# Kernel tuning notes

Measured on AMD Instinct MI355X. Metric: run time of the kernel, lower is better.

The kernel has to match this reference:

```python
import jax, jax.numpy as jnp
import numpy as np

D = 1024  # input_dim


def setup_inputs() -> dict:
    key = jax.random.key(0)
    ks = jax.random.split(key, 7)
    scale = 1.0 / np.sqrt(D)
    x = jax.random.normal(ks[0], (4, D, 2048), dtype=jnp.float32)
    Wq = jax.random.uniform(ks[1], (D, D), jnp.float32, -scale, scale)
    bq = jax.random.uniform(ks[2], (D,), jnp.float32, -scale, scale)
    Wk = jax.random.uniform(ks[3], (D, D), jnp.float32, -scale, scale)
    bk = jax.random.uniform(ks[4], (D,), jnp.float32, -scale, scale)
    Wv = jax.random.uniform(ks[5], (D, D), jnp.float32, -scale, scale)
    bv = jax.random.uniform(ks[6], (D,), jnp.float32, -scale, scale)
    return {"x": x, "Wq": Wq, "bq": bq, "Wk": Wk, "bk": bk, "Wv": Wv, "bv": bv}


def reference(x, Wq, bq, Wk, bk, Wv, bv):
    # x: [B, D, S] -> [B, S, D]
    xt = jnp.transpose(x, (0, 2, 1))
    # torch nn.Linear: y = x @ W^T + b
    q = jnp.einsum('bsd,ed->bse', xt, Wq) + bq
    k = jnp.einsum('bsd,ed->bse', xt, Wk) + bk
    v = jnp.einsum('bsd,ed->bse', xt, Wv) + bv
    scores = jnp.einsum('bse,bte->bst', q, k) / jnp.sqrt(jnp.float32(D))
    attn = jax.nn.softmax(scores, axis=2)
    out = jnp.einsum('bst,bte->bse', attn, v)  # [B, S, D]
    return out
```

## Files before the change

### kernel.cpp

```cpp
#include <hip/hip_runtime.h>
#include <stdint.h>

typedef unsigned short us16;
typedef unsigned short us8  __attribute__((ext_vector_type(8)));
typedef unsigned short us4v __attribute__((ext_vector_type(4)));
typedef __bf16         bf16x8 __attribute__((ext_vector_type(8)));
typedef float          f32x4  __attribute__((ext_vector_type(4)));

__device__ __forceinline__ us16 f2bf(float f) {
    union { float f; unsigned int u; } c; c.f = f;
    unsigned int u = (c.u + 0x7fffu + ((c.u >> 16) & 1u)) >> 16;
    return (us16)u;
}
__device__ __forceinline__ float bf2f(us16 h) {
    union { unsigned int u; float f; } c; c.u = ((unsigned int)h) << 16;
    return c.f;
}

__device__ __forceinline__ void async16(const us16* g, us16* l) {
    __builtin_amdgcn_global_load_lds(
        (const __attribute__((address_space(1))) unsigned int*)g,
        (__attribute__((address_space(3))) unsigned int*)l,
        16, 0, 0);
}

template <bool OUT_F32>
__device__ __forceinline__ void gemm_core(
        const us16* __restrict__ A, const us16* __restrict__ B,
        void* __restrict__ C, const float* __restrict__ bias, int biasmode,
        int M, int K, int x, int y, us16* lsA, us16* lsB) {
    const int m0 = x * 128, n0 = y * 128;
    const int tid = threadIdx.x;
    const int lane = tid & 63, wid = tid >> 6;
    const int l15 = lane & 15, quad = lane >> 4;
    const int wm = (wid & 1) * 64, wn = (wid >> 1) * 64;

    f32x4 acc[4][4] = {};

    const int srow = wid * 32 + (lane >> 3);
    const int sc8 = (lane & 7) ^ ((lane >> 3) & 7);
    const us16* Ap = A + (size_t)(m0 + srow) * K + sc8 * 8;
    const us16* Bp = B + (size_t)(n0 + srow) * K + sc8 * 8;
    us16* ldsAw = &lsA[(wid * 32) * 64];
    us16* ldsBw = &lsB[(wid * 32) * 64];

    for (int kb = 0; kb < K; kb += 64) {
        __syncthreads();
#pragma unroll
        for (int c = 0; c < 4; c++) {
            async16(Ap + kb + (size_t)(c * 8) * K, ldsAw + c * 8 * 64);
            async16(Bp + kb + (size_t)(c * 8) * K, ldsBw + c * 8 * 64);
        }
        __syncthreads();
#pragma unroll
        for (int ks = 0; ks < 2; ks++) {
            bf16x8 af[4], bfr[4];
#pragma unroll
            for (int i = 0; i < 4; i++) {
                const int ra = wm + i * 16 + l15;
                const int rb = wn + i * 16 + l15;
                const int pa = ((ks * 4 + quad) ^ (ra & 7)) * 8;
                const int pb = ((ks * 4 + quad) ^ (rb & 7)) * 8;
                af[i]  = *(const bf16x8*)(&lsA[ra * 64 + pa]);
                bfr[i] = *(const bf16x8*)(&lsB[rb * 64 + pb]);
            }
#pragma unroll
            for (int i = 0; i < 4; i++)
#pragma unroll
                for (int j = 0; j < 4; j++)
                    acc[i][j] = __builtin_amdgcn_mfma_f32_16x16x32_bf16(af[i], bfr[j], acc[i][j], 0, 0, 0);
        }
    }

#pragma unroll
    for (int i = 0; i < 4; i++) {
        const int mb = m0 + wm + i * 16 + quad * 4;
        float b0 = 0.f, b1 = 0.f, b2 = 0.f, b3 = 0.f;
        if (biasmode == 1) {
            float4 bv4 = *(const float4*)(bias + mb);
            b0 = bv4.x; b1 = bv4.y; b2 = bv4.z; b3 = bv4.w;
        }
#pragma unroll
        for (int j = 0; j < 4; j++) {
            const int n = n0 + wn + j * 16 + l15;
            const float bn = (biasmode == 2) ? bias[n] : 0.0f;
            f32x4 v = acc[i][j];
            const float o0 = v[0] + b0 + bn, o1 = v[1] + b1 + bn;
            const float o2 = v[2] + b2 + bn, o3 = v[3] + b3 + bn;
            if (OUT_F32) {
                float4 st; st.x = o0; st.y = o1; st.z = o2; st.w = o3;
                *(float4*)((float*)C + (size_t)n * M + mb) = st;
            } else {
                us4v st = { f2bf(o0), f2bf(o1), f2bf(o2), f2bf(o3) };
                *(us4v*)((us16*)C + (size_t)n * M + mb) = st;
            }
        }
    }
}

__device__ __forceinline__ void strip_xy(int lin, int gy, int& x, int& y) {
    const int within = lin & (4 * gy - 1);
    x = (lin / (4 * gy)) * 4 + (within & 3);
    y = within >> 2;
}

__global__ __launch_bounds__(256)
void prep(const float* __restrict__ x, us16* __restrict__ xt,
          const float* __restrict__ wq, const float* __restrict__ wk,
          const float* __restrict__ wv, us16* __restrict__ wb) {
    __shared__ us16 tile[64 * 65];
    const int id = blockIdx.x;
    const int t = threadIdx.x;
    if (id < 2048) {
        const int s0 = (id & 31) * 64, d0 = ((id >> 5) & 15) * 64, b = id >> 9;
        const float* xp = x + ((size_t)b * 1024 + d0) * 2048 + s0;
        const int r = t >> 4, c4 = t & 15;
#pragma unroll
        for (int i = 0; i < 4; i++) {
            float4 v = *(const float4*)(xp + (size_t)(r + 16 * i) * 2048 + c4 * 4);
            const int d = r + 16 * i;
            tile[(c4 * 4 + 0) * 65 + d] = f2bf(v.x);
            tile[(c4 * 4 + 1) * 65 + d] = f2bf(v.y);
            tile[(c4 * 4 + 2) * 65 + d] = f2bf(v.z);
            tile[(c4 * 4 + 3) * 65 + d] = f2bf(v.w);
        }
        __syncthreads();
        us16* op = xt + ((size_t)b * 2048 + s0) * 1024 + d0;
#pragma unroll
        for (int i = 0; i < 2; i++) {
            const int u = t + 256 * i;
            const int s = u >> 3, c8 = u & 7;
            us8 o;
#pragma unroll
            for (int j = 0; j < 8; j++) o[j] = tile[s * 65 + c8 * 8 + j];
            *(us8*)(op + (size_t)s * 1024 + c8 * 8) = o;
        }
    } else {
        const int cid = id - 2048;
        const int mb = cid >> 10;
        const float* src = (mb == 0) ? wq : (mb == 1) ? wk : wv;
        const size_t off = ((size_t)(cid & 1023) * 256 + t) * 4;
        float4 v = *(const float4*)(src + off);
        us4v o = { f2bf(v.x), f2bf(v.y), f2bf(v.z), f2bf(v.w) };
        *(us4v*)(wb + (size_t)mb * 1048576 + off) = o;
    }
}

__global__ __launch_bounds__(256)
void qkv(const us16* __restrict__ Wb, const us16* __restrict__ XT,
         us16* __restrict__ Qb, us16* __restrict__ Kb, us16* __restrict__ VT,
         const float* __restrict__ bq, const float* __restrict__ bk,
         const float* __restrict__ bv) {
    __shared__ us16 lsA[128 * 64];
    __shared__ us16 lsB[128 * 64];
    const int id = blockIdx.x;
    const long long sXT = 2097152;
    if (id < 1024) {
        const int z = id >> 7, zz = z & 3;
        const bool isK = z >= 4;
        int x, y; strip_xy(id & 127, 16, x, y);
        const us16* A = Wb + (isK ? 1048576 : 0);
        const us16* B = XT + (size_t)zz * sXT;
        us16* C = (isK ? Kb : Qb) + (size_t)zz * sXT;
        gemm_core<false>(A, B, (void*)C, isK ? bk : bq, 1, 1024, 1024, x, y, lsA, lsB);
    } else {
        const int id2 = id - 1024;
        const int z = id2 >> 7;
        int x, y; strip_xy(id2 & 127, 8, x, y);
        const us16* A = XT + (size_t)z * sXT;
        us16* C = VT + (size_t)z * sXT;
        gemm_core<false>(A, Wb + 2097152, (void*)C, bv, 2, 2048, 1024, x, y, lsA, lsB);
    }
}

__global__ __launch_bounds__(256)
void scores_k(const us16* __restrict__ Kb, const us16* __restrict__ Qb,
              us16* __restrict__ Sb) {
    __shared__ us16 lsA[128 * 64];
    __shared__ us16 lsB[128 * 64];
    const long long sXT = 2097152, sSS = 4194304;
    const int z = blockIdx.z;
    int x, y; strip_xy(blockIdx.x + 16 * blockIdx.y, 16, x, y);
    gemm_core<false>(Kb + (size_t)z * sXT, Qb + (size_t)z * sXT,
                     (void*)(Sb + (size_t)z * sSS), nullptr, 0,
                     2048, 1024, x, y, lsA, lsB);
}

__global__ __launch_bounds__(256)
void out_k(const us16* __restrict__ VT, const us16* __restrict__ Sb,
           float* __restrict__ out) {
    __shared__ us16 lsA[128 * 64];
    __shared__ us16 lsB[128 * 64];
    const long long sXT = 2097152, sSS = 4194304;
    const int z = blockIdx.z;
    int x, y; strip_xy(blockIdx.x + 8 * blockIdx.y, 16, x, y);
    gemm_core<true>(VT + (size_t)z * sXT, Sb + (size_t)z * sSS,
                    (void*)(out + (size_t)z * sXT), nullptr, 0,
                    1024, 2048, x, y, lsA, lsB);
}

__global__ __launch_bounds__(256)
void softmax_inplace(us16* __restrict__ S) {
    const float scale = 0.03125f;
    us16* p = S + (size_t)blockIdx.x * 2048;
    const int t = threadIdx.x;
    us8 v = *(const us8*)(p + t * 8);
    float x[8];
#pragma unroll
    for (int i = 0; i < 8; i++) x[i] = bf2f(v[i]) * scale;

    float m = x[0];
#pragma unroll
    for (int i = 1; i < 8; i++) m = fmaxf(m, x[i]);
#pragma unroll
    for (int off = 1; off < 64; off <<= 1) m = fmaxf(m, __shfl_xor(m, off, 64));
    __shared__ float red[4];
    __shared__ float red2[4];
    if ((t & 63) == 0) red[t >> 6] = m;
    __syncthreads();
    m = fmaxf(fmaxf(red[0], red[1]), fmaxf(red[2], red[3]));

    float s = 0.f;
#pragma unroll
    for (int i = 0; i < 8; i++) { x[i] = __expf(x[i] - m); s += x[i]; }
#pragma unroll
    for (int off = 1; off < 64; off <<= 1) s += __shfl_xor(s, off, 64);
    if ((t & 63) == 0) red2[t >> 6] = s;
    __syncthreads();
    s = red2[0] + red2[1] + red2[2] + red2[3];
    const float inv = 1.0f / s;

    us8 o;
#pragma unroll
    for (int i = 0; i < 8; i++) o[i] = f2bf(x[i] * inv);
    *(us8*)(p + t * 8) = o;
}

extern "C" void kernel_launch(void* const* d_in, const int* in_sizes, int n_in,
                              void* d_out, int out_size, void* d_ws, size_t ws_size,
                              hipStream_t stream) {
    const float* x  = (const float*)d_in[0];
    const float* Wq = (const float*)d_in[1];
    const float* bq = (const float*)d_in[2];
    const float* Wk = (const float*)d_in[3];
    const float* bk = (const float*)d_in[4];
    const float* Wv = (const float*)d_in[5];
    const float* bv = (const float*)d_in[6];
    float* out = (float*)d_out;
    char* ws = (char*)d_ws;

    const size_t SZ = 16777216;
    us16* Qb = (us16*)(ws);
    us16* Kb = (us16*)(ws + SZ);
    us16* VT = (us16*)(ws + 2 * SZ);
    us16* XT = (us16*)(ws + 3 * SZ);
    us16* Wb = (us16*)(ws + 4 * SZ);
    us16* Sb = (us16*)(ws + 3 * SZ);

    dim3 blk(256, 1, 1);

    prep<<<dim3(5120, 1, 1), blk, 0, stream>>>(x, XT, Wq, Wk, Wv, Wb);
    qkv<<<dim3(1536, 1, 1), blk, 0, stream>>>(Wb, XT, Qb, Kb, VT, bq, bk, bv);
    scores_k<<<dim3(16, 16, 4), blk, 0, stream>>>(Kb, Qb, Sb);
    softmax_inplace<<<dim3(8192, 1, 1), blk, 0, stream>>>(Sb);
    out_k<<<dim3(8, 16, 4), blk, 0, stream>>>(VT, Sb, out);
}
```

Baseline: 271.8 us.

## Double-buffer GEMM LDS tiles with 32-wide K steps to overlap loads and MFMA

Replaces the single-buffered 64-wide K tile with two 32-wide LDS buffers. The async global-to-LDS load of the next tile is issued before computing on the current one, so there is one barrier per step instead of a load-wait-compute pattern. The XOR swizzle is reworked for 32-element rows. This is meant to hide global load latency behind MFMA work, at the cost of twice as many barriers per unit of K and smaller per-step compute.

```diff
diff --git a/kernel.cpp b/kernel.cpp
--- a/kernel.cpp
+++ b/kernel.cpp
@@ -24,52 +24,67 @@
         16, 0, 0);
 }
 
+__device__ __forceinline__ void stage32(const us16* Ap, const us16* Bp,
+                                        us16* la, us16* lb, int K) {
+    async16(Ap, la);
+    async16(Ap + (size_t)16 * K, la + 16 * 32);
+    async16(Bp, lb);
+    async16(Bp + (size_t)16 * K, lb + 16 * 32);
+}
+
+__device__ __forceinline__ void compute32(const us16* La, const us16* Lb,
+        f32x4 (&acc)[4][4], int wm, int wn, int l15, int fsl) {
+    bf16x8 af[4], bfr[4];
+#pragma unroll
+    for (int i = 0; i < 4; i++) {
+        af[i]  = *(const bf16x8*)(&La[(wm + i * 16 + l15) * 32 + fsl]);
+        bfr[i] = *(const bf16x8*)(&Lb[(wn + i * 16 + l15) * 32 + fsl]);
+    }
+#pragma unroll
+    for (int i = 0; i < 4; i++)
+#pragma unroll
+        for (int j = 0; j < 4; j++)
+            acc[i][j] = __builtin_amdgcn_mfma_f32_16x16x32_bf16(af[i], bfr[j], acc[i][j], 0, 0, 0);
+}
+
 template <bool OUT_F32>
 __device__ __forceinline__ void gemm_core(
         const us16* __restrict__ A, const us16* __restrict__ B,
         void* __restrict__ C, const float* __restrict__ bias, int biasmode,
-        int M, int K, int x, int y, us16* lsA, us16* lsB) {
+        int M, int K, int x, int y, us16* ls) {
     const int m0 = x * 128, n0 = y * 128;
     const int tid = threadIdx.x;
     const int lane = tid & 63, wid = tid >> 6;
     const int l15 = lane & 15, quad = lane >> 4;
     const int wm = (wid & 1) * 64, wn = (wid >> 1) * 64;
+    const int fsl = (quad ^ ((l15 >> 1) & 3)) * 8;
 
     f32x4 acc[4][4] = {};
 
-    const int srow = wid * 32 + (lane >> 3);
-    const int sc8 = (lane & 7) ^ ((lane >> 3) & 7);
-    const us16* Ap = A + (size_t)(m0 + srow) * K + sc8 * 8;
-    const us16* Bp = B + (size_t)(n0 + srow) * K + sc8 * 8;
-    us16* ldsAw = &lsA[(wid * 32) * 64];
-    us16* ldsBw = &lsB[(wid * 32) * 64];
-
-    for (int kb = 0; kb < K; kb += 64) {
+    const int srow = lane >> 2;
+    const int sc4 = (lane & 3) ^ ((lane >> 3) & 3);
+    const us16* Ap = A + (size_t)(m0 + wid * 32 + srow) * K + sc4 * 8;
+    const us16* Bp = B + (size_t)(n0 + wid * 32 + srow) * K + sc4 * 8;
+    us16* lA0 = ls + (wid * 32) * 32;
+    us16* lB0 = ls + 4096 + (wid * 32) * 32;
+    us16* lA1 = lA0 + 8192;
+    us16* lB1 = lB0 + 8192;
+    const us16* La0 = ls;
+    const us16* Lb0 = ls + 4096;
+    const us16* La1 = ls + 8192;
+    const us16* Lb1 = ls + 12288;
+
+    stage32(Ap, Bp, lA0, lB0, K);
+    const int nIter = K >> 5;
+    int kb = 32;
+    for (int i = 0; i < nIter; i += 2) {
         __syncthreads();
-#pragma unroll
-        for (int c = 0; c < 4; c++) {
-            async16(Ap + kb + (size_t)(c * 8) * K, ldsAw + c * 8 * 64);
-            async16(Bp + kb + (size_t)(c * 8) * K, ldsBw + c * 8 * 64);
-        }
+        if (i + 1 < nIter) stage32(Ap + kb, Bp + kb, lA1, lB1, K);
+        compute32(La0, Lb0, acc, wm, wn, l15, fsl);
         __syncthreads();
-#pragma unroll
-        for (int ks = 0; ks < 2; ks++) {
-            bf16x8 af[4], bfr[4];
-#pragma unroll
-            for (int i = 0; i < 4; i++) {
-                const int ra = wm + i * 16 + l15;
-                const int rb = wn + i * 16 + l15;
-                const int pa = ((ks * 4 + quad) ^ (ra & 7)) * 8;
-                const int pb = ((ks * 4 + quad) ^ (rb & 7)) * 8;
-                af[i]  = *(const bf16x8*)(&lsA[ra * 64 + pa]);
-                bfr[i] = *(const bf16x8*)(&lsB[rb * 64 + pb]);
-            }
-#pragma unroll
-            for (int i = 0; i < 4; i++)
-#pragma unroll
-                for (int j = 0; j < 4; j++)
-                    acc[i][j] = __builtin_amdgcn_mfma_f32_16x16x32_bf16(af[i], bfr[j], acc[i][j], 0, 0, 0);
-        }
+        if (i + 2 < nIter) stage32(Ap + kb + 32, Bp + kb + 32, lA0, lB0, K);
+        compute32(La1, Lb1, acc, wm, wn, l15, fsl);
+        kb += 64;
     }
 
 #pragma unroll
@@ -151,8 +166,7 @@
          us16* __restrict__ Qb, us16* __restrict__ Kb, us16* __restrict__ VT,
          const float* __restrict__ bq, const float* __restrict__ bk,
          const float* __restrict__ bv) {
-    __shared__ us16 lsA[128 * 64];
-    __shared__ us16 lsB[128 * 64];
+    __shared__ us16 ls[16384];
     const int id = blockIdx.x;
     const long long sXT = 2097152;
     if (id < 1024) {
@@ -162,41 +176,39 @@
         const us16* A = Wb + (isK ? 1048576 : 0);
         const us16* B = XT + (size_t)zz * sXT;
         us16* C = (isK ? Kb : Qb) + (size_t)zz * sXT;
-        gemm_core<false>(A, B, (void*)C, isK ? bk : bq, 1, 1024, 1024, x, y, lsA, lsB);
+        gemm_core<false>(A, B, (void*)C, isK ? bk : bq, 1, 1024, 1024, x, y, ls);
     } else {
         const int id2 = id - 1024;
         const int z = id2 >> 7;
         int x, y; strip_xy(id2 & 127, 8, x, y);
         const us16* A = XT + (size_t)z * sXT;
         us16* C = VT + (size_t)z * sXT;
-        gemm_core<false>(A, Wb + 2097152, (void*)C, bv, 2, 2048, 1024, x, y, lsA, lsB);
+        gemm_core<false>(A, Wb + 2097152, (void*)C, bv, 2, 2048, 1024, x, y, ls);
     }
 }
 
 __global__ __launch_bounds__(256)
 void scores_k(const us16* __restrict__ Kb, const us16* __restrict__ Qb,
               us16* __restrict__ Sb) {
-    __shared__ us16 lsA[128 * 64];
-    __shared__ us16 lsB[128 * 64];
+    __shared__ us16 ls[16384];
     const long long sXT = 2097152, sSS = 4194304;
     const int z = blockIdx.z;
     int x, y; strip_xy(blockIdx.x + 16 * blockIdx.y, 16, x, y);
     gemm_core<false>(Kb + (size_t)z * sXT, Qb + (size_t)z * sXT,
                      (void*)(Sb + (size_t)z * sSS), nullptr, 0,
-                     2048, 1024, x, y, lsA, lsB);
+                     2048, 1024, x, y, ls);
 }
 
 __global__ __launch_bounds__(256)
 void out_k(const us16* __restrict__ VT, const us16* __restrict__ Sb,
            float* __restrict__ out) {
-    __shared__ us16 lsA[128 * 64];
-    __shared__ us16 lsB[128 * 64];
+    __shared__ us16 ls[16384];
     const long long sXT = 2097152, sSS = 4194304;
     const int z = blockIdx.z;
     int x, y; strip_xy(blockIdx.x + 8 * blockIdx.y, 16, x, y);
     gemm_core<true>(VT + (size_t)z * sXT, Sb + (size_t)z * sSS,
                     (void*)(out + (size_t)z * sXT), nullptr, 0,
-                    1024, 2048, x, y, lsA, lsB);
+                    1024, 2048, x, y, ls);
 }
 
 __global__ __launch_bounds__(256)
```

After: 290.7 us. 7.0% more time.

## Fuse softmax into scores epilogue and defer normalization to output GEMM

Applied to the files above, without the earlier changes.

Removes the separate softmax kernel. The scores GEMM epilogue now applies exp to the scaled scores, stores them as bf16, and accumulates per-row sums into a global buffer with atomics. The output GEMM divides by those sums in its epilogue. This saves a full read and write of the score matrix, but it drops the max subtraction, so exp could overflow for larger logits, and it adds a memset plus atomic traffic.

```diff
diff --git a/kernel.cpp b/kernel.cpp
--- a/kernel.cpp
+++ b/kernel.cpp
@@ -24,10 +24,11 @@
         16, 0, 0);
 }
 
-template <bool OUT_F32>
+template <int EPI>
 __device__ __forceinline__ void gemm_core(
         const us16* __restrict__ A, const us16* __restrict__ B,
-        void* __restrict__ C, const float* __restrict__ bias, int biasmode,
+        void* __restrict__ C, const float* __restrict__ bias,
+        float* __restrict__ L,
         int M, int K, int x, int y, us16* lsA, us16* lsB) {
     const int m0 = x * 128, n0 = y * 128;
     const int tid = threadIdx.x;
@@ -72,26 +73,58 @@
         }
     }
 
+    if (EPI == 2) {
+        const float scale = 0.03125f;
+        float rs[4] = {0.f, 0.f, 0.f, 0.f};
+#pragma unroll
+        for (int i = 0; i < 4; i++) {
+            const int mb = m0 + wm + i * 16 + quad * 4;
+#pragma unroll
+            for (int j = 0; j < 4; j++) {
+                const int n = n0 + wn + j * 16 + l15;
+                f32x4 v = acc[i][j];
+                const float e0 = __expf(v[0] * scale), e1 = __expf(v[1] * scale);
+                const float e2 = __expf(v[2] * scale), e3 = __expf(v[3] * scale);
+                rs[j] += (e0 + e1) + (e2 + e3);
+                us4v st = { f2bf(e0), f2bf(e1), f2bf(e2), f2bf(e3) };
+                *(us4v*)((us16*)C + (size_t)n * M + mb) = st;
+            }
+        }
+#pragma unroll
+        for (int j = 0; j < 4; j++) {
+            rs[j] += __shfl_xor(rs[j], 16, 64);
+            rs[j] += __shfl_xor(rs[j], 32, 64);
+        }
+        if (quad == 0) {
+#pragma unroll
+            for (int j = 0; j < 4; j++)
+                atomicAdd(&L[n0 + wn + j * 16 + l15], rs[j]);
+        }
+        return;
+    }
+
 #pragma unroll
     for (int i = 0; i < 4; i++) {
         const int mb = m0 + wm + i * 16 + quad * 4;
         float b0 = 0.f, b1 = 0.f, b2 = 0.f, b3 = 0.f;
-        if (biasmode == 1) {
+        if (EPI == 0) {
             float4 bv4 = *(const float4*)(bias + mb);
             b0 = bv4.x; b1 = bv4.y; b2 = bv4.z; b3 = bv4.w;
         }
 #pragma unroll
         for (int j = 0; j < 4; j++) {
             const int n = n0 + wn + j * 16 + l15;
-            const float bn = (biasmode == 2) ? bias[n] : 0.0f;
             f32x4 v = acc[i][j];
-            const float o0 = v[0] + b0 + bn, o1 = v[1] + b1 + bn;
-            const float o2 = v[2] + b2 + bn, o3 = v[3] + b3 + bn;
-            if (OUT_F32) {
-                float4 st; st.x = o0; st.y = o1; st.z = o2; st.w = o3;
+            if (EPI == 3) {
+                const float inv = 1.0f / L[n];
+                float4 st;
+                st.x = v[0] * inv; st.y = v[1] * inv;
+                st.z = v[2] * inv; st.w = v[3] * inv;
                 *(float4*)((float*)C + (size_t)n * M + mb) = st;
             } else {
-                us4v st = { f2bf(o0), f2bf(o1), f2bf(o2), f2bf(o3) };
+                const float bn = (EPI == 1) ? bias[n] : 0.0f;
+                us4v st = { f2bf(v[0] + b0 + bn), f2bf(v[1] + b1 + bn),
+                            f2bf(v[2] + b2 + bn), f2bf(v[3] + b3 + bn) };
                 *(us4v*)((us16*)C + (size_t)n * M + mb) = st;
             }
         }
@@ -162,78 +195,41 @@
         const us16* A = Wb + (isK ? 1048576 : 0);
         const us16* B = XT + (size_t)zz * sXT;
         us16* C = (isK ? Kb : Qb) + (size_t)zz * sXT;
-        gemm_core<false>(A, B, (void*)C, isK ? bk : bq, 1, 1024, 1024, x, y, lsA, lsB);
+        gemm_core<0>(A, B, (void*)C, isK ? bk : bq, nullptr, 1024, 1024, x, y, lsA, lsB);
     } else {
         const int id2 = id - 1024;
         const int z = id2 >> 7;
         int x, y; strip_xy(id2 & 127, 8, x, y);
         const us16* A = XT + (size_t)z * sXT;
         us16* C = VT + (size_t)z * sXT;
-        gemm_core<false>(A, Wb + 2097152, (void*)C, bv, 2, 2048, 1024, x, y, lsA, lsB);
+        gemm_core<1>(A, Wb + 2097152, (void*)C, bv, nullptr, 2048, 1024, x, y, lsA, lsB);
     }
 }
 
 __global__ __launch_bounds__(256)
 void scores_k(const us16* __restrict__ Kb, const us16* __restrict__ Qb,
-              us16* __restrict__ Sb) {
+              us16* __restrict__ Sb, float* __restrict__ L) {
     __shared__ us16 lsA[128 * 64];
     __shared__ us16 lsB[128 * 64];
     const long long sXT = 2097152, sSS = 4194304;
     const int z = blockIdx.z;
     int x, y; strip_xy(blockIdx.x + 16 * blockIdx.y, 16, x, y);
-    gemm_core<false>(Kb + (size_t)z * sXT, Qb + (size_t)z * sXT,
-                     (void*)(Sb + (size_t)z * sSS), nullptr, 0,
-                     2048, 1024, x, y, lsA, lsB);
+    gemm_core<2>(Kb + (size_t)z * sXT, Qb + (size_t)z * sXT,
+                 (void*)(Sb + (size_t)z * sSS), nullptr, L + z * 2048,
+                 2048, 1024, x, y, lsA, lsB);
 }
 
 __global__ __launch_bounds__(256)
 void out_k(const us16* __restrict__ VT, const us16* __restrict__ Sb,
-           float* __restrict__ out) {
+           float* __restrict__ L, float* __restrict__ out) {
     __shared__ us16 lsA[128 * 64];
     __shared__ us16 lsB[128 * 64];
     const long long sXT = 2097152, sSS = 4194304;
     const int z = blockIdx.z;
     int x, y; strip_xy(blockIdx.x + 8 * blockIdx.y, 16, x, y);
-    gemm_core<true>(VT + (size_t)z * sXT, Sb + (size_t)z * sSS,
-                    (void*)(out + (size_t)z * sXT), nullptr, 0,
-                    1024, 2048, x, y, lsA, lsB);
-}
-
-__global__ __launch_bounds__(256)
-void softmax_inplace(us16* __restrict__ S) {
-    const float scale = 0.03125f;
-    us16* p = S + (size_t)blockIdx.x * 2048;
-    const int t = threadIdx.x;
-    us8 v = *(const us8*)(p + t * 8);
-    float x[8];
-#pragma unroll
-    for (int i = 0; i < 8; i++) x[i] = bf2f(v[i]) * scale;
-
-    float m = x[0];
-#pragma unroll
-    for (int i = 1; i < 8; i++) m = fmaxf(m, x[i]);
-#pragma unroll
-    for (int off = 1; off < 64; off <<= 1) m = fmaxf(m, __shfl_xor(m, off, 64));
-    __shared__ float red[4];
-    __shared__ float red2[4];
-    if ((t & 63) == 0) red[t >> 6] = m;
-    __syncthreads();
-    m = fmaxf(fmaxf(red[0], red[1]), fmaxf(red[2], red[3]));
-
-    float s = 0.f;
-#pragma unroll
-    for (int i = 0; i < 8; i++) { x[i] = __expf(x[i] - m); s += x[i]; }
-#pragma unroll
-    for (int off = 1; off < 64; off <<= 1) s += __shfl_xor(s, off, 64);
-    if ((t & 63) == 0) red2[t >> 6] = s;
-    __syncthreads();
-    s = red2[0] + red2[1] + red2[2] + red2[3];
-    const float inv = 1.0f / s;
-
-    us8 o;
-#pragma unroll
-    for (int i = 0; i < 8; i++) o[i] = f2bf(x[i] * inv);
-    *(us8*)(p + t * 8) = o;
+    gemm_core<3>(VT + (size_t)z * sXT, Sb + (size_t)z * sSS,
+                 (void*)(out + (size_t)z * sXT), nullptr, L + z * 2048,
+                 1024, 2048, x, y, lsA, lsB);
 }
 
 extern "C" void kernel_launch(void* const* d_in, const int* in_sizes, int n_in,
@@ -256,12 +252,13 @@
     us16* XT = (us16*)(ws + 3 * SZ);
     us16* Wb = (us16*)(ws + 4 * SZ);
     us16* Sb = (us16*)(ws + 3 * SZ);
+    float* Lb = (float*)(ws + 5 * SZ);
 
     dim3 blk(256, 1, 1);
 
+    hipMemsetAsync(Lb, 0, 4 * 2048 * sizeof(float), stream);
     prep<<<dim3(5120, 1, 1), blk, 0, stream>>>(x, XT, Wq, Wk, Wv, Wb);
     qkv<<<dim3(1536, 1, 1), blk, 0, stream>>>(Wb, XT, Qb, Kb, VT, bq, bk, bv);
-    scores_k<<<dim3(16, 16, 4), blk, 0, stream>>>(Kb, Qb, Sb);
-    softmax_inplace<<<dim3(8192, 1, 1), blk, 0, stream>>>(Sb);
-    out_k<<<dim3(8, 16, 4), blk, 0, stream>>>(VT, Sb, out);
-}
+    scores_k<<<dim3(16, 16, 4), blk, 0, stream>>>(Kb, Qb, Sb, Lb);
+    out_k<<<dim3(8, 16, 4), blk, 0, stream>>>(VT, Sb, Lb, out);
+}
```

New measurement: 246.3 us. 9.4% less time.
